# Kernel optimization log

Hardware: AMD Instinct MI355X
Metric: run time of the kernel (lower is better)

The kernel has to match this reference:

```python
import jax, jax.numpy as jnp
import numpy as np

N, E = 50000, 200000
SIZES = [16, 32, 16]
EDIM = 8
EPS = 1e-5


def setup_inputs() -> dict:
    key = jax.random.key(0)
    ks = jax.random.split(key, 16)
    inp = {
        "x": jax.random.normal(ks[0], (N, SIZES[0]), jnp.float32),
        "edge_attr": jax.random.normal(ks[1], (E, EDIM), jnp.float32),
        "edge_index": jax.random.randint(ks[2], (2, E), 0, N, dtype=jnp.int32),
    }
    ki = 3
    for l in range(2):
        fin, fout = SIZES[l], SIZES[l + 1]
        m = fin * fout
        # xavier-ish init matching torch.nn.init.xavier_uniform_ scales
        inp[f"W1_{l}"] = jax.random.normal(ks[ki], (EDIM, m), jnp.float32) / np.float32(np.sqrt(EDIM)); ki += 1
        inp[f"b1_{l}"] = jnp.zeros((m,), jnp.float32)
        inp[f"W2_{l}"] = jax.random.normal(ks[ki], (m, m), jnp.float32) * np.float32(0.01 / np.sqrt(m)); ki += 1
        inp[f"b2_{l}"] = jnp.zeros((m,), jnp.float32)
        inp[f"root_{l}"] = jax.random.normal(ks[ki], (fin, fout), jnp.float32) / np.float32(np.sqrt(fin)); ki += 1
        inp[f"bias_{l}"] = jnp.zeros((fout,), jnp.float32)
        inp[f"gamma_{l}"] = jnp.ones((fout,), jnp.float32)
        inp[f"beta_{l}"] = jnp.zeros((fout,), jnp.float32)
    return inp


def _lrelu(v):
    return jnp.where(v >= 0, v, 0.01 * v)


def _nnconv(x, src, dst, edge_attr, W1, b1, W2, b2, root, bias, fin, fout):
    # edge MLP -> per-edge weight matrix [E, fin, fout]
    h = _lrelu(edge_attr @ W1 + b1) @ W2 + b2
    h = h.reshape(-1, fin, fout)
    # gather source node features, tiny per-edge matmul
    msg = jnp.einsum('ei,eio->eo', x[src], h)  # [E, fout]
    # scatter-mean aggregate at destination nodes
    agg = jax.ops.segment_sum(msg, dst, num_segments=N)
    deg = jax.ops.segment_sum(jnp.ones((msg.shape[0],), msg.dtype), dst, num_segments=N)
    agg = agg / jnp.maximum(deg, 1.0)[:, None]
    return agg + x @ root + bias


def _bn(v, gamma, beta):
    # BatchNorm1d (training mode: batch stats, biased variance)
    mu = v.mean(0)
    var = v.var(0)
    return (v - mu) * jax.lax.rsqrt(var + EPS) * gamma + beta


def reference(x, edge_attr,
              W1_0, b1_0, W2_0, b2_0, root_0, bias_0, gamma_0, beta_0,
              W1_1, b1_1, W2_1, b2_1, root_1, bias_1, gamma_1, beta_1,
              edge_index):
    src, dst = edge_index[0], edge_index[1]
    h = _nnconv(x, src, dst, edge_attr, W1_0, b1_0, W2_0, b2_0, root_0, bias_0, SIZES[0], SIZES[1])
    h = _lrelu(_bn(h, gamma_0, beta_0))
    h = _nnconv(h, src, dst, edge_attr, W1_1, b1_1, W2_1, b2_1, root_1, bias_1, SIZES[1], SIZES[2])
    return _bn(h, gamma_1, beta_1)
```

## Files before the change

### kernel.cpp

```cpp
#include <hip/hip_runtime.h>
#include <hip/hip_bf16.h>

typedef __attribute__((ext_vector_type(4))) float f32x4;
typedef __attribute__((ext_vector_type(8))) short s16x8;
typedef __attribute__((ext_vector_type(4))) int int4v;

#define DEVI __device__ __forceinline__

constexpr int NN = 50000;
constexpr int NE = 200000;
constexpr float BN_EPS = 1e-5f;

DEVI float bfbits2f(unsigned v) { union { unsigned u; float f; } t; t.u = v << 16; return t.f; }
DEVI float lrelu_f(float v) { return v >= 0.f ? v : 0.01f * v; }

__global__ void k_transpose_w2(const float* __restrict__ A0, const float* __restrict__ A1,
                               __hip_bfloat16* __restrict__ T0, __hip_bfloat16* __restrict__ T1) {
  const float* W2 = blockIdx.y ? A1 : A0;
  __hip_bfloat16* W2T = blockIdx.y ? T1 : T0;
  __shared__ float tile[32][33];
  int bx = blockIdx.x % 16, by = blockIdx.x / 16;
  int t = threadIdx.x;
  int r = t / 32, c = t % 32;
  for (int rr = r; rr < 32; rr += 8)
    tile[rr][c] = W2[(size_t)(by * 32 + rr) * 512 + bx * 32 + c];
  __syncthreads();
  for (int rr = r; rr < 32; rr += 8)
    W2T[(size_t)(bx * 32 + rr) * 512 + by * 32 + c] = __float2bfloat16(tile[c][rr]);
}

__global__ void k_transpose_w1(const float* __restrict__ A0, const float* __restrict__ A1,
                               __hip_bfloat16* __restrict__ T0, __hip_bfloat16* __restrict__ T1) {
  const float* W1 = blockIdx.y ? A1 : A0;
  __hip_bfloat16* W1T = blockIdx.y ? T1 : T0;
  int tid = blockIdx.x * 256 + threadIdx.x;
  if (tid < 8 * 512) {
    int k = tid / 512, n = tid % 512;
    W1T[n * 8 + k] = __float2bfloat16(W1[tid]);
  }
}

__global__ void k_count(const int* __restrict__ dst, int* __restrict__ cnt) {
  int e = blockIdx.x * 256 + threadIdx.x;
  if (e < NE) atomicAdd(&cnt[dst[e]], 1);
}

constexpr int SCAN_ELEMS = 1024;
__global__ void k_scan1(const int* __restrict__ cnt, int* __restrict__ base, int* __restrict__ aux, int n) {
  __shared__ int sw[256];
  int b = blockIdx.x, t = threadIdx.x;
  int i0 = b * SCAN_ELEMS + t * 4;
  int v[4]; int s = 0;
  #pragma unroll
  for (int j = 0; j < 4; j++) { int idx = i0 + j; v[j] = (idx < n) ? cnt[idx] : 0; s += v[j]; }
  sw[t] = s; __syncthreads();
  for (int d = 1; d < 256; d <<= 1) {
    int val = (t >= d) ? sw[t - d] : 0;
    __syncthreads();
    sw[t] += val;
    __syncthreads();
  }
  int run = (t > 0) ? sw[t - 1] : 0;
  #pragma unroll
  for (int j = 0; j < 4; j++) { int idx = i0 + j; if (idx < n) base[idx] = run; run += v[j]; }
  if (t == 255) aux[b] = sw[255];
}

__global__ void k_scan2(int* aux, int nb) {
  if (threadIdx.x == 0 && blockIdx.x == 0) {
    int run = 0;
    for (int i = 0; i < nb; i++) { int v = aux[i]; aux[i] = run; run += v; }
  }
}

__global__ void k_scan3(int* __restrict__ base, int* __restrict__ cursor, const int* __restrict__ aux, int n) {
  int i = blockIdx.x * 256 + threadIdx.x;
  if (i < n) { int v = base[i] + aux[i / SCAN_ELEMS]; base[i] = v; cursor[i] = v; }
}

__global__ void k_place(const int* __restrict__ dst, int* __restrict__ cursor, int* __restrict__ perm) {
  int e = blockIdx.x * 256 + threadIdx.x;
  if (e < NE) { int p = atomicAdd(&cursor[dst[e]], 1); perm[p] = e; }
}

template <int FIN, int FOUT>
__global__ __launch_bounds__(256, 4)
void k_edge(const float* __restrict__ x, const float* __restrict__ ea,
            const int* __restrict__ srcI,
            const __hip_bfloat16* __restrict__ W1T, const float* __restrict__ b1,
            const __hip_bfloat16* __restrict__ W2T, const float* __restrict__ b2,
            __hip_bfloat16* __restrict__ msgb)
{
  static_assert(FOUT == 32 || FOUT == 16, "");
  constexpr int TM = 256;
  constexpr int CG = 32;
  constexpr int NCGI = 16;
  constexpr int KH = 64;
  constexpr int NSW = 8;
  constexpr int NOT = FOUT / 16;

  __shared__ __align__(16) char gbuf[4][4096];
  __shared__ __align__(16) char bbuf[2][CG * 128];
  __shared__ __align__(16) __hip_bfloat16 xlt[FIN][TM];

  const int tid = threadIdx.x;
  const int lane = tid & 63, w = tid >> 6;
  const int l15 = lane & 15, l4 = lane >> 4;
  const int e0 = blockIdx.x * TM;
  const int rem = min(TM, NE - e0);
  const int wrow0 = w * 64;

  union { s16x8 v; int i4[4]; } earow;
  {
    int er = e0 + min(tid, rem - 1);
    float4 v0 = *(const float4*)(ea + (size_t)er * 8);
    float4 v1 = *(const float4*)(ea + (size_t)er * 8 + 4);
    __hip_bfloat16* p = (__hip_bfloat16*)&earow;
    p[0] = __float2bfloat16(v0.x); p[1] = __float2bfloat16(v0.y);
    p[2] = __float2bfloat16(v0.z); p[3] = __float2bfloat16(v0.w);
    p[4] = __float2bfloat16(v1.x); p[5] = __float2bfloat16(v1.y);
    p[6] = __float2bfloat16(v1.z); p[7] = __float2bfloat16(v1.w);
    int s = srcI[er];
    #pragma unroll
    for (int q = 0; q < FIN / 4; q++) {
      float4 xv4 = *(const float4*)(x + (size_t)s * FIN + q * 4);
      xlt[q * 4 + 0][tid] = __float2bfloat16(xv4.x);
      xlt[q * 4 + 1][tid] = __float2bfloat16(xv4.y);
      xlt[q * 4 + 2][tid] = __float2bfloat16(xv4.z);
      xlt[q * 4 + 3][tid] = __float2bfloat16(xv4.w);
    }
  }

  f32x4 msg[4][NOT];
  #pragma unroll
  for (int rt = 0; rt < 4; rt++)
    #pragma unroll
    for (int ot = 0; ot < NOT; ot++) msg[rt][ot] = (f32x4)(0.f);

  s16x8 af[2][4];
  const int st_col = tid >> 3, st_s = tid & 7;
  const int st_dst = st_col * 128 + ((st_s ^ (st_col & 7)) << 4);
  const char* W2Tb = (const char*)W2T;
  char* gme = gbuf[w];

  for (int sw = 0; sw < NSW; ++sw) {
    int4v sr = *(const int4v*)(W2Tb + (size_t)st_col * 1024 + sw * 128 + st_s * 16);

    #pragma unroll
    for (int h = 0; h < 2; ++h) {
      s16x8 afe[2];
      #pragma unroll
      for (int rt2 = 0; rt2 < 2; rt2++) {
        union { s16x8 v; int i4[4]; } t2;
        #pragma unroll
        for (int q = 0; q < 4; q++) t2.i4[q] = __shfl(earow.i4[q], (h * 2 + rt2) * 16 + l15);
        afe[rt2] = (lane < 16) ? t2.v : (s16x8)0;
      }
      #pragma unroll
      for (int ct = 0; ct < 4; ++ct) {
        int c = sw * KH + ct * 16 + l15;
        s16x8 bw = *(const s16x8*)(W1T + c * 8);
        bw = (lane < 16) ? bw : (s16x8)0;
        float b1v = b1[c];
        #pragma unroll
        for (int rt2 = 0; rt2 < 2; rt2++) {
          f32x4 d = __builtin_amdgcn_mfma_f32_16x16x32_bf16(afe[rt2], bw, (f32x4)(0.f), 0, 0, 0);
          #pragma unroll
          for (int r = 0; r < 4; r++) {
            int rloc = rt2 * 16 + l4 * 4 + r;
            float gv = d[r] + b1v;
            gv = gv >= 0.f ? gv : 0.01f * gv;
            int byt = (rloc * 128 + (ct * 16 + l15) * 2) ^ ((rloc & 7) << 4);
            *(__hip_bfloat16*)(gme + byt) = __float2bfloat16(gv);
          }
        }
      }
      #pragma unroll
      for (int rt2 = 0; rt2 < 2; rt2++)
        #pragma unroll
        for (int kst = 0; kst < 2; kst++) {
          int rloc = rt2 * 16 + l15;
          int byt = (rloc * 128 + (kst * 64 + l4 * 16)) ^ ((rloc & 7) << 4);
          af[kst][h * 2 + rt2] = *(const s16x8*)(gme + byt);
        }
    }
    #pragma unroll
    for (int kst = 0; kst < 2; kst++)
      #pragma unroll
      for (int rt = 0; rt < 4; rt++)
        asm volatile("" : "+v"(af[kst][rt]));

    *(int4v*)(&bbuf[0][st_dst]) = sr;
    __syncthreads();

    for (int cgi = 0; cgi < NCGI; ++cgi) {
      if (cgi + 1 < NCGI)
        sr = *(const int4v*)(W2Tb + (size_t)((cgi + 1) * CG + st_col) * 1024 + sw * 128 + st_s * 16);
      const char* bb = bbuf[cgi & 1];

      #pragma unroll
      for (int ct = 0; ct < 2; ++ct) {
        const int c = ct * 16 + l15;
        const int cbase = c * 128;
        const int csw = (c & 7);
        f32x4 acc[4];
        acc[0] = (f32x4)(0.f); acc[1] = (f32x4)(0.f);
        acc[2] = (f32x4)(0.f); acc[3] = (f32x4)(0.f);
        #pragma unroll
        for (int kst = 0; kst < 2; ++kst) {
          const s16x8 bw = *(const s16x8*)(bb + cbase + (((kst * 4 + l4) ^ csw) << 4));
          #pragma unroll
          for (int rt = 0; rt < 4; rt++)
            acc[rt] = __builtin_amdgcn_mfma_f32_16x16x32_bf16(af[kst][rt], bw, acc[rt], 0, 0, 0);
        }
        float b2v = (sw == 0) ? b2[cgi * CG + ct * 16 + l15] : 0.f;
        const int iv = (FOUT == 32) ? cgi : (cgi * 2 + ct);
        const int ot = (FOUT == 32) ? ct : 0;
        #pragma unroll
        for (int rt = 0; rt < 4; rt++) {
          int rbase = wrow0 + rt * 16 + l4 * 4;
          ushort4 xv = *(const ushort4*)(&xlt[iv][rbase]);
          msg[rt][ot][0] += bfbits2f(xv.x) * (acc[rt][0] + b2v);
          msg[rt][ot][1] += bfbits2f(xv.y) * (acc[rt][1] + b2v);
          msg[rt][ot][2] += bfbits2f(xv.z) * (acc[rt][2] + b2v);
          msg[rt][ot][3] += bfbits2f(xv.w) * (acc[rt][3] + b2v);
        }
      }
      if (cgi + 1 < NCGI)
        *(int4v*)(&bbuf[(cgi + 1) & 1][st_dst]) = sr;
      __syncthreads();
    }
  }

  #pragma unroll
  for (int rt = 0; rt < 4; rt++)
    #pragma unroll
    for (int r = 0; r < 4; r++) {
      int row = wrow0 + rt * 16 + l4 * 4 + r;
      if (row < rem) {
        #pragma unroll
        for (int ot = 0; ot < NOT; ot++)
          msgb[(size_t)(e0 + row) * FOUT + ot * 16 + l15] = __float2bfloat16(msg[rt][ot][r]);
      }
    }
}

template <int FIN, int FOUT>
__global__ void k_node_agg(const __hip_bfloat16* __restrict__ msgb, const int* __restrict__ perm,
                           const int* __restrict__ base,
                           const float* __restrict__ x,
                           const float* __restrict__ root,
                           const float* __restrict__ bias,
                           float* __restrict__ h)
{
  __shared__ float rl[FIN * FOUT];
  constexpr int NPB = 256 / FOUT;
  int t = threadIdx.x;
  for (int i = t; i < FIN * FOUT; i += 256) rl[i] = root[i];
  __syncthreads();
  int n = blockIdx.x * NPB + t / FOUT;
  int o = t % FOUT;
  if (n >= NN) return;
  int s = base[n];
  int e = (n + 1 < NN) ? base[n + 1] : NE;
  float sum = 0.f;
  for (int j = s; j < e; j++)
    sum += __bfloat162float(msgb[(size_t)perm[j] * FOUT + o]);
  float acc = sum / fmaxf((float)(e - s), 1.f) + bias[o];
  #pragma unroll
  for (int i = 0; i < FIN; i++)
    acc += x[(size_t)n * FIN + i] * rl[i * FOUT + o];
  h[(size_t)n * FOUT + o] = acc;
}

template <int FOUT>
__global__ void k_stats(const float* __restrict__ h, float* __restrict__ ssum, float* __restrict__ ssq) {
  constexpr int RPB = 256 / FOUT;
  int t = threadIdx.x;
  int o = t % FOUT, rr = t / FOUT;
  float v = 0.f, v2 = 0.f;
  for (int r = blockIdx.x * RPB + rr; r < NN; r += gridDim.x * RPB) {
    float y = h[(size_t)r * FOUT + o];
    v += y; v2 += y * y;
  }
  #pragma unroll
  for (int d = FOUT; d < 64; d <<= 1) { v += __shfl_xor(v, d); v2 += __shfl_xor(v2, d); }
  __shared__ float sv[4][32], sq[4][32];
  int wv = t >> 6, ln = t & 63;
  if (ln < FOUT) { sv[wv][ln] = v; sq[wv][ln] = v2; }
  __syncthreads();
  if (t < FOUT) {
    float a = 0.f, b = 0.f;
    #pragma unroll
    for (int w2 = 0; w2 < 4; w2++) { a += sv[w2][t]; b += sq[w2][t]; }
    atomicAdd(&ssum[t], a);
    atomicAdd(&ssq[t], b);
  }
}

template <int FOUT, bool LRELU>
__global__ void k_bn(const float* __restrict__ h, const float* __restrict__ ssum,
                     const float* __restrict__ ssq, const float* __restrict__ gamma,
                     const float* __restrict__ beta, float* __restrict__ out)
{
  int idx = blockIdx.x * 256 + threadIdx.x;
  if (idx * 4 >= NN * FOUT) return;
  float4 v = *(const float4*)(h + (size_t)idx * 4);
  float r[4] = {v.x, v.y, v.z, v.w};
  #pragma unroll
  for (int j = 0; j < 4; j++) {
    int o = (idx * 4 + j) % FOUT;
    float mu = ssum[o] * (1.f / NN);
    float var = ssq[o] * (1.f / NN) - mu * mu;
    float sc = rsqrtf(var + BN_EPS) * gamma[o];
    float y = (r[j] - mu) * sc + beta[o];
    if (LRELU) y = lrelu_f(y);
    r[j] = y;
  }
  *(float4*)(out + (size_t)idx * 4) = make_float4(r[0], r[1], r[2], r[3]);
}

extern "C" void kernel_launch(void* const* d_in, const int* in_sizes, int n_in,
                              void* d_out, int out_size, void* d_ws, size_t ws_size,
                              hipStream_t stream)
{
  const float* x0    = (const float*)d_in[0];
  const float* ea    = (const float*)d_in[1];
  const int*   ei    = (const int*)d_in[2];
  const float* W1_0  = (const float*)d_in[3];
  const float* b1_0  = (const float*)d_in[4];
  const float* W2_0  = (const float*)d_in[5];
  const float* b2_0  = (const float*)d_in[6];
  const float* root0 = (const float*)d_in[7];
  const float* bias0 = (const float*)d_in[8];
  const float* gam0  = (const float*)d_in[9];
  const float* bet0  = (const float*)d_in[10];
  const float* W1_1  = (const float*)d_in[11];
  const float* b1_1  = (const float*)d_in[12];
  const float* W2_1  = (const float*)d_in[13];
  const float* b2_1  = (const float*)d_in[14];
  const float* root1 = (const float*)d_in[15];
  const float* bias1 = (const float*)d_in[16];
  const float* gam1  = (const float*)d_in[17];
  const float* bet1  = (const float*)d_in[18];
  const int* srcI = ei;
  const int* dstI = ei + NE;

  char* ws = (char*)d_ws;
  size_t off = 0;
  auto alloc = [&](size_t bytes) { char* p = ws + off; off += (bytes + 255) & ~(size_t)255; return p; };
  int*   cnt   = (int*)alloc(50048 * 4);
  float* ssum0 = (float*)alloc(32 * 4);
  float* ssq0  = (float*)alloc(32 * 4);
  float* ssum1 = (float*)alloc(16 * 4);
  float* ssq1  = (float*)alloc(16 * 4);
  size_t zero_bytes = off;
  int*   base   = (int*)alloc(50048 * 4);
  int*   cursor = (int*)alloc(50048 * 4);
  int*   aux    = (int*)alloc(64 * 4);
  int*   perm   = (int*)alloc((size_t)NE * 4);
  __hip_bfloat16* msgb = (__hip_bfloat16*)alloc((size_t)NE * 32 * 2);
  float* h0 = (float*)alloc((size_t)NN * 32 * 4);
  float* h1 = (float*)alloc((size_t)NN * 16 * 4);
  float* x1 = (float*)alloc((size_t)NN * 32 * 4);
  __hip_bfloat16* W2T0 = (__hip_bfloat16*)alloc(512 * 512 * 2);
  __hip_bfloat16* W2T1 = (__hip_bfloat16*)alloc(512 * 512 * 2);
  __hip_bfloat16* W1T0 = (__hip_bfloat16*)alloc(512 * 8 * 2);
  __hip_bfloat16* W1T1 = (__hip_bfloat16*)alloc(512 * 8 * 2);

  hipMemsetAsync(d_ws, 0, zero_bytes, stream);

  k_transpose_w2<<<dim3(256, 2), 256, 0, stream>>>(W2_0, W2_1, W2T0, W2T1);
  k_transpose_w1<<<dim3(16, 2), 256, 0, stream>>>(W1_0, W1_1, W1T0, W1T1);

  constexpr int NSB = (NN + SCAN_ELEMS - 1) / SCAN_ELEMS;
  k_count<<<(NE + 255) / 256, 256, 0, stream>>>(dstI, cnt);
  k_scan1<<<NSB, 256, 0, stream>>>(cnt, base, aux, NN);
  k_scan2<<<1, 64, 0, stream>>>(aux, NSB);
  k_scan3<<<(NN + 255) / 256, 256, 0, stream>>>(base, cursor, aux, NN);
  k_place<<<(NE + 255) / 256, 256, 0, stream>>>(dstI, cursor, perm);

  constexpr int TM = 256;
  k_edge<16, 32><<<(NE + TM - 1) / TM, 256, 0, stream>>>(x0, ea, srcI, W1T0, b1_0, W2T0, b2_0, msgb);
  k_node_agg<16, 32><<<(NN + 7) / 8, 256, 0, stream>>>(msgb, perm, base, x0, root0, bias0, h0);
  k_stats<32><<<128, 256, 0, stream>>>(h0, ssum0, ssq0);
  k_bn<32, true><<<((NN * 32 / 4) + 255) / 256, 256, 0, stream>>>(h0, ssum0, ssq0, gam0, bet0, x1);

  k_edge<32, 16><<<(NE + TM - 1) / TM, 256, 0, stream>>>(x1, ea, srcI, W1T1, b1_1, W2T1, b2_1, msgb);
  k_node_agg<32, 16><<<(NN + 15) / 16, 256, 0, stream>>>(msgb, perm, base, x1, root1, bias1, h1);
  k_stats<16><<<128, 256, 0, stream>>>(h1, ssum1, ssq1);
  k_bn<16, false><<<((NN * 16 / 4) + 255) / 256, 256, 0, stream>>>(h1, ssum1, ssq1, gam1, bet1, (float*)d_out);
}
```

Baseline: 472.8 us.

## Double the K-chunk per stage in edge kernel to halve barrier-synced passes

Raises the K chunk of the per-edge W2 GEMM from 64 to 128, so there are half as many outer stages and half as many W2 staging/__syncthreads rounds. Each thread now holds twice the A fragments and stages two W2 vectors per step. The b2 bias is folded into the accumulator's initial value, and the xlt row stride is padded to avoid LDS bank conflicts. This raises register and LDS pressure, so launch bounds drop to 3 blocks per SM, which lowers occupancy.

```diff
diff --git a/kernel.cpp b/kernel.cpp
--- a/kernel.cpp
+++ b/kernel.cpp
@@ -84,7 +84,7 @@
 }
 
 template <int FIN, int FOUT>
-__global__ __launch_bounds__(256, 4)
+__global__ __launch_bounds__(256, 3)
 void k_edge(const float* __restrict__ x, const float* __restrict__ ea,
             const int* __restrict__ srcI,
             const __hip_bfloat16* __restrict__ W1T, const float* __restrict__ b1,
@@ -95,13 +95,14 @@
   constexpr int TM = 256;
   constexpr int CG = 32;
   constexpr int NCGI = 16;
-  constexpr int KH = 64;
-  constexpr int NSW = 8;
+  constexpr int KH = 128;
+  constexpr int NSW = 4;
   constexpr int NOT = FOUT / 16;
-
+  constexpr int XLDS = TM + 8;
+
+  __shared__ __align__(16) char bbuf[2][CG * 256];
   __shared__ __align__(16) char gbuf[4][4096];
-  __shared__ __align__(16) char bbuf[2][CG * 128];
-  __shared__ __align__(16) __hip_bfloat16 xlt[FIN][TM];
+  __shared__ __align__(16) __hip_bfloat16 xlt[FIN][XLDS];
 
   const int tid = threadIdx.x;
   const int lane = tid & 63, w = tid >> 6;
@@ -137,97 +138,116 @@
     #pragma unroll
     for (int ot = 0; ot < NOT; ot++) msg[rt][ot] = (f32x4)(0.f);
 
-  s16x8 af[2][4];
+  s16x8 af[4][4];
   const int st_col = tid >> 3, st_s = tid & 7;
-  const int st_dst = st_col * 128 + ((st_s ^ (st_col & 7)) << 4);
   const char* W2Tb = (const char*)W2T;
   char* gme = gbuf[w];
+  int4v sr0, sr1;
 
   for (int sw = 0; sw < NSW; ++sw) {
-    int4v sr = *(const int4v*)(W2Tb + (size_t)st_col * 1024 + sw * 128 + st_s * 16);
-
-    #pragma unroll
-    for (int h = 0; h < 2; ++h) {
+    {
+      const char* gp = W2Tb + (size_t)st_col * 1024 + sw * 256;
+      sr0 = *(const int4v*)(gp + st_s * 16);
+      sr1 = *(const int4v*)(gp + (st_s + 8) * 16);
+    }
+    #pragma unroll
+    for (int hr = 0; hr < 2; ++hr) {
       s16x8 afe[2];
       #pragma unroll
       for (int rt2 = 0; rt2 < 2; rt2++) {
         union { s16x8 v; int i4[4]; } t2;
         #pragma unroll
-        for (int q = 0; q < 4; q++) t2.i4[q] = __shfl(earow.i4[q], (h * 2 + rt2) * 16 + l15);
+        for (int q = 0; q < 4; q++) t2.i4[q] = __shfl(earow.i4[q], (hr * 2 + rt2) * 16 + l15);
         afe[rt2] = (lane < 16) ? t2.v : (s16x8)0;
       }
       #pragma unroll
-      for (int ct = 0; ct < 4; ++ct) {
-        int c = sw * KH + ct * 16 + l15;
-        s16x8 bw = *(const s16x8*)(W1T + c * 8);
-        bw = (lane < 16) ? bw : (s16x8)0;
-        float b1v = b1[c];
-        #pragma unroll
-        for (int rt2 = 0; rt2 < 2; rt2++) {
-          f32x4 d = __builtin_amdgcn_mfma_f32_16x16x32_bf16(afe[rt2], bw, (f32x4)(0.f), 0, 0, 0);
+      for (int hk = 0; hk < 2; ++hk) {
+        #pragma unroll
+        for (int ct = 0; ct < 4; ct++) {
+          int c = sw * KH + hk * 64 + ct * 16 + l15;
+          s16x8 bw = *(const s16x8*)(W1T + c * 8);
+          bw = (lane < 16) ? bw : (s16x8)0;
+          float b1v = b1[c];
           #pragma unroll
-          for (int r = 0; r < 4; r++) {
-            int rloc = rt2 * 16 + l4 * 4 + r;
-            float gv = d[r] + b1v;
-            gv = gv >= 0.f ? gv : 0.01f * gv;
-            int byt = (rloc * 128 + (ct * 16 + l15) * 2) ^ ((rloc & 7) << 4);
-            *(__hip_bfloat16*)(gme + byt) = __float2bfloat16(gv);
+          for (int rt2 = 0; rt2 < 2; rt2++) {
+            f32x4 d = __builtin_amdgcn_mfma_f32_16x16x32_bf16(afe[rt2], bw, (f32x4)(0.f), 0, 0, 0);
+            #pragma unroll
+            for (int r = 0; r < 4; r++) {
+              int rloc = rt2 * 16 + l4 * 4 + r;
+              float gv = d[r] + b1v;
+              gv = gv >= 0.f ? gv : 0.01f * gv;
+              int byt = (rloc * 128 + (ct * 16 + l15) * 2) ^ ((rloc & 7) << 4);
+              *(__hip_bfloat16*)(gme + byt) = __float2bfloat16(gv);
+            }
           }
         }
-      }
-      #pragma unroll
-      for (int rt2 = 0; rt2 < 2; rt2++)
-        #pragma unroll
-        for (int kst = 0; kst < 2; kst++) {
-          int rloc = rt2 * 16 + l15;
-          int byt = (rloc * 128 + (kst * 64 + l4 * 16)) ^ ((rloc & 7) << 4);
-          af[kst][h * 2 + rt2] = *(const s16x8*)(gme + byt);
-        }
+        #pragma unroll
+        for (int rt2 = 0; rt2 < 2; rt2++)
+          #pragma unroll
+          for (int kk = 0; kk < 2; kk++) {
+            int rloc = rt2 * 16 + l15;
+            int byt = (rloc * 128 + (kk * 32 + l4 * 8) * 2) ^ ((rloc & 7) << 4);
+            af[hk * 2 + kk][hr * 2 + rt2] = *(const s16x8*)(gme + byt);
+          }
+      }
     }
     #pragma unroll
-    for (int kst = 0; kst < 2; kst++)
+    for (int kst = 0; kst < 4; kst++)
       #pragma unroll
       for (int rt = 0; rt < 4; rt++)
         asm volatile("" : "+v"(af[kst][rt]));
 
-    *(int4v*)(&bbuf[0][st_dst]) = sr;
+    *(int4v*)(&bbuf[0][st_col * 256 + ((st_s ^ (st_col & 7)) << 4)]) = sr0;
+    *(int4v*)(&bbuf[0][st_col * 256 + (((st_s + 8) ^ (st_col & 7)) << 4)]) = sr1;
     __syncthreads();
 
     for (int cgi = 0; cgi < NCGI; ++cgi) {
-      if (cgi + 1 < NCGI)
-        sr = *(const int4v*)(W2Tb + (size_t)((cgi + 1) * CG + st_col) * 1024 + sw * 128 + st_s * 16);
+      if (cgi + 1 < NCGI) {
+        const char* gp = W2Tb + (size_t)((cgi + 1) * CG + st_col) * 1024 + sw * 256;
+        sr0 = *(const int4v*)(gp + st_s * 16);
+        sr1 = *(const int4v*)(gp + (st_s + 8) * 16);
+      }
       const char* bb = bbuf[cgi & 1];
 
       #pragma unroll
       for (int ct = 0; ct < 2; ++ct) {
         const int c = ct * 16 + l15;
-        const int cbase = c * 128;
-        const int csw = (c & 7);
+        const int cbase = c * 256;
+        const int csw = c & 7;
         f32x4 acc[4];
-        acc[0] = (f32x4)(0.f); acc[1] = (f32x4)(0.f);
-        acc[2] = (f32x4)(0.f); acc[3] = (f32x4)(0.f);
-        #pragma unroll
-        for (int kst = 0; kst < 2; ++kst) {
-          const s16x8 bw = *(const s16x8*)(bb + cbase + (((kst * 4 + l4) ^ csw) << 4));
+        if (sw == 0) {
+          float b2v = b2[cgi * CG + c];
+          acc[0] = (f32x4)(b2v); acc[1] = (f32x4)(b2v);
+          acc[2] = (f32x4)(b2v); acc[3] = (f32x4)(b2v);
+        } else {
+          acc[0] = (f32x4)(0.f); acc[1] = (f32x4)(0.f);
+          acc[2] = (f32x4)(0.f); acc[3] = (f32x4)(0.f);
+        }
+        #pragma unroll
+        for (int kst = 0; kst < 4; ++kst) {
+          const int slot = kst * 4 + l4;
+          const s16x8 bw = *(const s16x8*)(bb + cbase + ((slot ^ csw) << 4));
           #pragma unroll
           for (int rt = 0; rt < 4; rt++)
             acc[rt] = __builtin_amdgcn_mfma_f32_16x16x32_bf16(af[kst][rt], bw, acc[rt], 0, 0, 0);
         }
-        float b2v = (sw == 0) ? b2[cgi * CG + ct * 16 + l15] : 0.f;
         const int iv = (FOUT == 32) ? cgi : (cgi * 2 + ct);
         const int ot = (FOUT == 32) ? ct : 0;
         #pragma unroll
         for (int rt = 0; rt < 4; rt++) {
           int rbase = wrow0 + rt * 16 + l4 * 4;
           ushort4 xv = *(const ushort4*)(&xlt[iv][rbase]);
-          msg[rt][ot][0] += bfbits2f(xv.x) * (acc[rt][0] + b2v);
-          msg[rt][ot][1] += bfbits2f(xv.y) * (acc[rt][1] + b2v);
-          msg[rt][ot][2] += bfbits2f(xv.z) * (acc[rt][2] + b2v);
-          msg[rt][ot][3] += bfbits2f(xv.w) * (acc[rt][3] + b2v);
+          msg[rt][ot][0] += bfbits2f(xv.x) * acc[rt][0];
+          msg[rt][ot][1] += bfbits2f(xv.y) * acc[rt][1];
+          msg[rt][ot][2] += bfbits2f(xv.z) * acc[rt][2];
+          msg[rt][ot][3] += bfbits2f(xv.w) * acc[rt][3];
         }
       }
-      if (cgi + 1 < NCGI)
-        *(int4v*)(&bbuf[(cgi + 1) & 1][st_dst]) = sr;
+      if (cgi + 1 < NCGI) {
+        char* bw2 = bbuf[(cgi + 1) & 1];
+        *(int4v*)(&bw2[st_col * 256 + ((st_s ^ (st_col & 7)) << 4)]) = sr0;
+        *(int4v*)(&bw2[st_col * 256 + (((st_s + 8) ^ (st_col & 7)) << 4)]) = sr1;
+      }
       __syncthreads();
     }
   }
```

Result: slower. 484.8 us (+2.5%).
